# Optimization experiments

Hardware: AMD Instinct MI355X
Metric: run time of the kernel (lower is better)

Reference implementation:

```python
import jax, jax.numpy as jnp
import numpy as np

DN = ('NCHW', 'OIHW', 'NCHW')
A, NC = 3, 80  # num_anchors, num_classes


def conv(x, w, b, pad=1):
    y = jax.lax.conv_general_dilated(x, w, (1, 1), [(pad, pad), (pad, pad)], dimension_numbers=DN)
    return y + b[None, :, None, None]


def up2(x):
    return jnp.repeat(jnp.repeat(x, 2, axis=2), 2, axis=3)


def gen_anchors():
    # AnchorGenerator: sizes per level, 3 aspect ratios, 1 scale, stride=2**(i+3)
    sizes = [32.0, 64.0, 128.0]
    ars = [0.5, 1.0, 2.0]
    hw = [(64, 64), (32, 32), (16, 16)]
    out = []
    for i, ((h, w), bs) in enumerate(zip(hw, sizes)):
        stride = 2.0 ** (i + 3)
        base = np.array([[-bs * np.sqrt(a) / 2, -bs / np.sqrt(a) / 2,
                          bs * np.sqrt(a) / 2, bs / np.sqrt(a) / 2] for a in ars], dtype=np.float32)
        sx = np.arange(w, dtype=np.float32) * stride
        sy = np.arange(h, dtype=np.float32) * stride
        yy, xx = np.meshgrid(sy, sx, indexing='ij')  # torch.meshgrid default 'ij'
        shifts = np.stack([xx.ravel(), yy.ravel(), xx.ravel(), yy.ravel()], axis=1)
        anc = (base[None, :, :] + shifts[:, None, :]).reshape(-1, 4)
        out.append(anc)
    return jnp.asarray(np.concatenate(out, axis=0))


def setup_inputs() -> dict:
    key = jax.random.key(0)
    ks = jax.random.split(key, 32)
    def w(k, o, i, kh, kw):
        return jax.random.normal(k, (o, i, kh, kw), jnp.float32) * 0.02
    B = 8
    inp = {
        'feat3': jax.random.normal(ks[0], (B, 512, 64, 64), jnp.float32),
        'feat4': jax.random.normal(ks[1], (B, 1024, 32, 32), jnp.float32),
        'feat5': jax.random.normal(ks[2], (B, 2048, 16, 16), jnp.float32),
        # FPN lateral 1x1 convs
        'lw0': w(ks[3], 256, 512, 1, 1),  'lb0': jnp.zeros(256, jnp.float32),
        'lw1': w(ks[4], 256, 1024, 1, 1), 'lb1': jnp.zeros(256, jnp.float32),
        'lw2': w(ks[5], 256, 2048, 1, 1), 'lb2': jnp.zeros(256, jnp.float32),
        # FPN 3x3 output convs
        'fw0': w(ks[6], 256, 256, 3, 3), 'fb0': jnp.zeros(256, jnp.float32),
        'fw1': w(ks[7], 256, 256, 3, 3), 'fb1': jnp.zeros(256, jnp.float32),
        'fw2': w(ks[8], 256, 256, 3, 3), 'fb2': jnp.zeros(256, jnp.float32),
        # cls tower (shared across levels)
        'cw0': w(ks[9], 256, 256, 3, 3),  'cb0': jnp.zeros(256, jnp.float32),
        'cw1': w(ks[10], 256, 256, 3, 3), 'cb1': jnp.zeros(256, jnp.float32),
        'cw2': w(ks[11], A * NC, 256, 3, 3), 'cb2': jnp.zeros(A * NC, jnp.float32),
        # reg tower (shared across levels)
        'rw0': w(ks[12], 256, 256, 3, 3), 'rb0': jnp.zeros(256, jnp.float32),
        'rw1': w(ks[13], 256, 256, 3, 3), 'rb1': jnp.zeros(256, jnp.float32),
        'rw2': w(ks[14], A * 4, 256, 3, 3), 'rb2': jnp.zeros(A * 4, jnp.float32),
    }
    return inp


def _tower(f, w0, b0, w1, b1, w2, b2):
    x = jax.nn.relu(conv(f, w0, b0))
    x = jax.nn.relu(conv(x, w1, b1))
    return conv(x, w2, b2)


def reference(feat3, feat4, feat5,
              lw0, lb0, lw1, lb1, lw2, lb2,
              fw0, fb0, fw1, fb1, fw2, fb2,
              cw0, cb0, cw1, cb1, cw2, cb2,
              rw0, rb0, rw1, rb1, rw2, rb2):
    B = feat3.shape[0]
    # FPN: lateral 1x1 convs + top-down nearest upsample fusion + 3x3 convs
    l0 = conv(feat3, lw0, lb0, pad=0)
    l1 = conv(feat4, lw1, lb1, pad=0)
    l2 = conv(feat5, lw2, lb2, pad=0)
    l1 = l1 + up2(l2)
    l0 = l0 + up2(l1)
    feats = [conv(l0, fw0, fb0), conv(l1, fw1, fb1), conv(l2, fw2, fb2)]
    cls_list, reg_list = [], []
    for f in feats:
        c = _tower(f, cw0, cb0, cw1, cb1, cw2, cb2)  # [B, A*NC, H, W]
        r = _tower(f, rw0, rb0, rw1, rb1, rw2, rb2)  # [B, A*4, H, W]
        H, W = c.shape[2], c.shape[3]
        # view(B, A, C, HW).permute(0, 3, 1, 2) -> [B, HW, A, C]
        c = c.reshape(B, A, NC, H * W).transpose(0, 3, 1, 2)
        r = r.reshape(B, A, 4, H * W).transpose(0, 3, 1, 2)
        cls_list.append(c.reshape(B, H * W, A * NC))
        reg_list.append(r.reshape(B, H * W, A * 4))
    cls_all = jnp.concatenate(cls_list, axis=1)   # [B, 5376, 240]
    reg_all = jnp.concatenate(reg_list, axis=1)   # [B, 5376, 12]
    out = jnp.concatenate([cls_all, reg_all], axis=-1)  # [B, 5376, 252]
    anchors = gen_anchors()  # [16128, 4]
    return out, anchors
```

## Files before the change

### kernel.cpp

```cpp
#include <hip/hip_runtime.h>

typedef __bf16 bf16_t;
typedef __bf16 bf16x8 __attribute__((ext_vector_type(8)));
typedef float f32x4 __attribute__((ext_vector_type(4)));

__device__ inline void gl_lds16(const bf16_t* g, bf16_t* l) {
  __builtin_amdgcn_global_load_lds(
      (const __attribute__((address_space(1))) void*)g,
      (__attribute__((address_space(3))) void*)l, 16, 0, 0);
}

__global__ __launch_bounds__(256)
void nchw_to_nhwc(const float* __restrict__ in, bf16_t* __restrict__ out,
                  int C, int HW) {
  __shared__ float tile[64][65];
  const int n = blockIdx.z;
  const int c0 = blockIdx.y * 64, p0 = blockIdx.x * 64;
  const int t = threadIdx.x;
  const float* src = in + ((size_t)n * C + c0) * HW + p0;
  const int cl = t >> 6;
  const int pl = t & 63;
#pragma unroll
  for (int i = 0; i < 16; ++i)
    tile[cl + i * 4][pl] = src[(size_t)(cl + i * 4) * HW + pl];
  __syncthreads();
  bf16_t* dst = out + ((size_t)n * HW + p0) * C + c0;
  const int pc = t >> 6;
  const int cc = t & 63;
#pragma unroll
  for (int i = 0; i < 16; ++i)
    dst[(size_t)(pc + i * 4) * C + cc] = (bf16_t)tile[cc][pc + i * 4];
}

struct WSrc {
  const float *lw0, *lw1, *lw2;
  const float* w9[9];
  int O9[9];
};
__global__ __launch_bounds__(256)
void weight_prep(WSrc s, bf16_t* __restrict__ LWT0, bf16_t* __restrict__ LWT1,
                 bf16_t* __restrict__ LWT2, bf16_t* __restrict__ W33) {
  int idx = blockIdx.x * 256 + threadIdx.x;
  if (idx < 131072) { LWT0[idx] = (bf16_t)s.lw0[idx]; return; }
  if (idx < 393216) { int i = idx - 131072; LWT1[i] = (bf16_t)s.lw1[i]; return; }
  if (idx < 917504) { int i = idx - 393216; LWT2[i] = (bf16_t)s.lw2[i]; return; }
  int t2 = idx - 917504;
  if (t2 >= 9 * 589824) return;
  int sgi = t2 / 589824;
  int r = t2 - sgi * 589824;
  int kid = r >> 16;
  int rem = r & 65535;
  int o = rem >> 8, ci = rem & 255;
  const float* src = s.w9[sgi];
  int O = s.O9[sgi];
  W33[t2] = (o < O) ? (bf16_t)src[((size_t)o * 256 + ci) * 9 + kid] : (bf16_t)0.0f;
}

__global__ __launch_bounds__(256)
void up2_add_p(bf16_t* __restrict__ dst, const bf16_t* __restrict__ src,
               int lw, int lhw, int dWp, int dNs, int sWp, int sNs, int tot8) {
  int idx = blockIdx.x * 256 + threadIdx.x;
  if (idx >= tot8) return;
  const int c8 = idx & 31;
  const int pos = idx >> 5;
  const int n = pos >> lhw;
  const int rem = pos & ((1 << lhw) - 1);
  const int y = rem >> lw, x = rem & ((1 << lw) - 1);
  bf16_t* d = dst + ((size_t)n * dNs + (y + 1) * dWp + (x + 1)) * 256 + c8 * 8;
  const bf16_t* sp = src + ((size_t)n * sNs + ((y >> 1) + 1) * sWp + ((x >> 1) + 1)) * 256 + c8 * 8;
  bf16x8 dv = *(bf16x8*)d;
  bf16x8 sv = *(const bf16x8*)sp;
#pragma unroll
  for (int k = 0; k < 8; ++k) dv[k] = (bf16_t)((float)dv[k] + (float)sv[k]);
  *(bf16x8*)d = dv;
}

struct Job1 {
  const bf16_t* A;
  const bf16_t* Wt;
  const float* bias;
  bf16_t* outb;
  int mtiles, lw, lhw, oWp, onstride, Cin, pad0, pad1;
};
struct Job1Pack { Job1 j[3]; };

__global__ __launch_bounds__(256, 2)
void conv1_batch(Job1Pack jp) {
  __shared__ __align__(16) bf16_t As[2][128 * 32];
  __shared__ __align__(16) bf16_t Bs[2][128 * 32];
  int b = blockIdx.x, ji = 0;
#pragma unroll 1
  for (; ji < 2; ++ji) {
    int sz = jp.j[ji].mtiles * 2;
    if (b < sz) break;
    b -= sz;
  }
  const Job1 J = jp.j[ji];
  const int nt = b & 1, mt = b >> 1;
  const int m0 = mt * 128, n0 = nt * 128;
  const int t = threadIdx.x, l = t & 63, w = t >> 6;
  const int W = 1 << J.lw, HW = 1 << J.lhw;
  const int sr = l >> 2, seg = (l & 3) * 8;
  const bf16_t* aptr[2];
  const bf16_t* bptr[2];
  int lrow[2];
#pragma unroll
  for (int q = 0; q < 2; ++q) {
    const int r = w * 32 + q * 16 + sr;
    aptr[q] = J.A + (size_t)(m0 + r) * J.Cin + seg;
    bptr[q] = J.Wt + (size_t)(n0 + r) * J.Cin + seg;
    lrow[q] = (w * 32 + q * 16) * 32;
  }
  const int fr = l & 15, qd = l >> 4;
  const int wm = (w & 1) * 64, wn = (w >> 1) * 64;

  f32x4 acc[4][4];
#pragma unroll
  for (int i = 0; i < 4; ++i)
#pragma unroll
    for (int j = 0; j < 4; ++j)
#pragma unroll
      for (int r = 0; r < 4; ++r) acc[i][j][r] = 0.0f;

  auto stage = [&](int buf, int kk) {
#pragma unroll
    for (int q = 0; q < 2; ++q) {
      gl_lds16(aptr[q] + (size_t)kk * 32, &As[buf][lrow[q]]);
      gl_lds16(bptr[q] + (size_t)kk * 32, &Bs[buf][lrow[q]]);
    }
  };

  stage(0, 0);

  const int kiters = J.Cin >> 5;
#pragma unroll 1
  for (int kk = 0; kk < kiters; ++kk) {
    const int cur = kk & 1;
    __syncthreads();
    if (kk + 1 < kiters) stage(cur ^ 1, kk + 1);
    bf16x8 af[4], bfv[4];
#pragma unroll
    for (int i = 0; i < 4; ++i)
      af[i] = *(const bf16x8*)&As[cur][(wm + i * 16 + fr) * 32 + qd * 8];
#pragma unroll
    for (int j = 0; j < 4; ++j)
      bfv[j] = *(const bf16x8*)&Bs[cur][(wn + j * 16 + fr) * 32 + qd * 8];
#pragma unroll
    for (int i = 0; i < 4; ++i)
#pragma unroll
      for (int j = 0; j < 4; ++j)
        acc[i][j] = __builtin_amdgcn_mfma_f32_16x16x32_bf16(af[i], bfv[j],
                                                            acc[i][j], 0, 0, 0);
  }

#pragma unroll
  for (int i = 0; i < 4; ++i) {
    const int mrow = m0 + wm + i * 16 + qd * 4;
#pragma unroll
    for (int j = 0; j < 4; ++j) {
      const int co = n0 + wn + j * 16 + fr;
      const float bv = J.bias[co];
#pragma unroll
      for (int r = 0; r < 4; ++r) {
        float v = acc[i][j][r] + bv;
        const int m = mrow + r;
        const int n = m >> J.lhw, hw = m & (HW - 1);
        const int y = hw >> J.lw, x = hw & (W - 1);
        J.outb[((size_t)n * J.onstride + (y + 1) * J.oWp + (x + 1)) * 256 + co] =
            (bf16_t)v;
      }
    }
  }
}

struct Job3 {
  const bf16_t* A;
  const bf16_t* Wt;
  const float* bias;
  bf16_t* outb;
  int mtiles, ntiles, lw, lhw, Wp, nsA, oWp, onstride;
  int relu, Cout, pos_off, ch_off, use_outf, nAr, Pc, pad_;
};
struct Job3Pack { Job3 j[6]; };

__global__ __launch_bounds__(256, 2)
void conv3_batch(Job3Pack jp, float* __restrict__ outf) {
  __shared__ __align__(16) bf16_t As[320 * 32];
  __shared__ __align__(16) bf16_t Bs[2][384 * 32];
  int b = blockIdx.x, ji = 0;
#pragma unroll 1
  for (; ji < 5; ++ji) {
    int sz = jp.j[ji].mtiles * jp.j[ji].ntiles;
    if (b < sz) break;
    b -= sz;
  }
  const Job3 J = jp.j[ji];
  const int nt = (J.ntiles == 2) ? (b & 1) : 0;
  const int mt = (J.ntiles == 2) ? (b >> 1) : b;
  const int m0 = mt * 128, n0 = nt * 128;
  const int t = threadIdx.x, l = t & 63, w = t >> 6;
  const int W = 1 << J.lw, HW = 1 << J.lhw;
  const int sr = l >> 2, seg = (l & 3) * 8;
  const int fr = l & 15, qd = l >> 4;
  const int wm = (w & 1) * 64, wn = (w >> 1) * 64;
  const int wrow = w * 16 + sr;

  const int n_img = m0 >> J.lhw;
  const int Y0 = (m0 & (HW - 1)) >> J.lw;
  const bf16_t* Ag = J.A + ((size_t)n_img * J.nsA + (size_t)Y0 * J.Wp) * 256;

  int apix[4];
#pragma unroll
  for (int i = 0; i < 4; ++i) {
    const int m = wm + i * 16 + fr;
    const int y = m >> J.lw, x = m & (W - 1);
    apix[i] = ((y + 1) * J.Wp + (x + 1)) * 32 + qd * 8;
  }

  f32x4 acc[4][4];
#pragma unroll
  for (int i = 0; i < 4; ++i)
#pragma unroll
    for (int j = 0; j < 4; ++j)
#pragma unroll
      for (int r = 0; r < 4; ++r) acc[i][j][r] = 0.0f;

  auto stageB = [&](int buf, int ky, int cboff) {
#pragma unroll
    for (int r = 0; r < 6; ++r) {
      const int R = r * 64 + wrow;
      const int tp = R >> 7, co = R & 127;
      gl_lds16(J.Wt + (size_t)(ky * 3 + tp) * 65536 +
                   (size_t)(n0 + co) * 256 + cboff + seg,
               &Bs[buf][(r * 64 + w * 16) * 32]);
    }
  };
  auto stageA = [&](int cboff) {
#pragma unroll 1
    for (int r = 0; r < J.nAr; ++r) {
      int p = r * 64 + wrow;
      p = (p < J.Pc) ? p : (J.Pc - 1);
      gl_lds16(Ag + (size_t)p * 256 + cboff + seg,
               &As[(r * 64 + w * 16) * 32]);
    }
  };

  stageA(0);
  stageB(0, 0, 0);

  int cb = 0, ky = 0;
#pragma unroll 1
  for (int p = 0; p < 24; ++p) {
    const int cur = p & 1;
    __syncthreads();
    if (p < 23) {
      int kyn = ky + 1, cbn = cb;
      if (kyn == 3) { kyn = 0; cbn = cb + 1; }
      stageB(cur ^ 1, kyn, cbn * 32);
    }
    const bool aB = (ky == 2) && (cb < 7);
    const int dyoff = (ky - 1) * J.Wp * 32;
#pragma unroll
    for (int kx = 0; kx < 3; ++kx) {
      const int d = dyoff + (kx - 1) * 32;
      bf16x8 af[4], bfv[4];
#pragma unroll
      for (int i = 0; i < 4; ++i)
        af[i] = *(const bf16x8*)&As[apix[i] + d];
#pragma unroll
      for (int j = 0; j < 4; ++j)
        bfv[j] = *(const bf16x8*)&Bs[cur][(kx * 128 + wn + j * 16 + fr) * 32 + qd * 8];
      if (kx == 2 && aB) {
        asm volatile("s_waitcnt lgkmcnt(0)" ::: "memory");
        __builtin_amdgcn_sched_barrier(0);
        __builtin_amdgcn_s_barrier();
        __builtin_amdgcn_sched_barrier(0);
        stageA((cb + 1) * 32);
      }
#pragma unroll
      for (int i = 0; i < 4; ++i)
#pragma unroll
        for (int j = 0; j < 4; ++j)
          acc[i][j] = __builtin_amdgcn_mfma_f32_16x16x32_bf16(af[i], bfv[j],
                                                              acc[i][j], 0, 0, 0);
    }
    ky = (ky == 2) ? 0 : ky + 1;
    if (ky == 0) ++cb;
  }

#pragma unroll
  for (int i = 0; i < 4; ++i) {
    const int mrow = m0 + wm + i * 16 + qd * 4;
#pragma unroll
    for (int j = 0; j < 4; ++j) {
      const int co = n0 + wn + j * 16 + fr;
      if (co < J.Cout) {
        const float bv = J.bias[co];
#pragma unroll
        for (int r = 0; r < 4; ++r) {
          float v = acc[i][j][r] + bv;
          if (J.relu) v = fmaxf(v, 0.0f);
          const int m = mrow + r;
          const int n = m >> J.lhw, hw = m & (HW - 1);
          if (J.use_outf) {
            outf[((size_t)n * 5376 + J.pos_off + hw) * 252 + J.ch_off + co] = v;
          } else {
            const int y = hw >> J.lw, x = hw & (W - 1);
            J.outb[((size_t)n * J.onstride + (y + 1) * J.oWp + (x + 1)) * 256 + co] =
                (bf16_t)v;
          }
        }
      }
    }
  }
}

__global__ __launch_bounds__(256)
void anchors_k(float* __restrict__ out) {
  int r = blockIdx.x * 256 + threadIdx.x;
  if (r >= 16128) return;
  int local, w, stride;
  float bs;
  if (r < 12288)      { local = r;          w = 64; stride = 8;  bs = 32.f;  }
  else if (r < 15360) { local = r - 12288;  w = 32; stride = 16; bs = 64.f;  }
  else                { local = r - 15360;  w = 16; stride = 32; bs = 128.f; }
  const int a = local % 3;
  const int s = local / 3;
  const int y = s / w, x = s - y * w;
  const float ar = (a == 0) ? 0.5f : (a == 1) ? 1.0f : 2.0f;
  const float sq = sqrtf(ar);
  const float hw_ = bs * sq * 0.5f, hh = bs / sq * 0.5f;
  const float cx = (float)x * (float)stride, cy = (float)y * (float)stride;
  out[(size_t)r * 4 + 0] = cx - hw_;
  out[(size_t)r * 4 + 1] = cy - hh;
  out[(size_t)r * 4 + 2] = cx + hw_;
  out[(size_t)r * 4 + 3] = cy + hh;
}

extern "C" void kernel_launch(void* const* d_in, const int* in_sizes, int n_in,
                              void* d_out, int out_size, void* d_ws, size_t ws_size,
                              hipStream_t stream) {
  const float* feat3 = (const float*)d_in[0];
  const float* feat4 = (const float*)d_in[1];
  const float* feat5 = (const float*)d_in[2];
  const float* lw0 = (const float*)d_in[3];  const float* lb0 = (const float*)d_in[4];
  const float* lw1 = (const float*)d_in[5];  const float* lb1 = (const float*)d_in[6];
  const float* lw2 = (const float*)d_in[7];  const float* lb2 = (const float*)d_in[8];
  const float* fw0 = (const float*)d_in[9];  const float* fb0 = (const float*)d_in[10];
  const float* fw1 = (const float*)d_in[11]; const float* fb1 = (const float*)d_in[12];
  const float* fw2 = (const float*)d_in[13]; const float* fb2 = (const float*)d_in[14];
  const float* cw0 = (const float*)d_in[15]; const float* cb0 = (const float*)d_in[16];
  const float* cw1 = (const float*)d_in[17]; const float* cb1 = (const float*)d_in[18];
  const float* cw2 = (const float*)d_in[19]; const float* cb2 = (const float*)d_in[20];
  const float* rw0 = (const float*)d_in[21]; const float* rb0 = (const float*)d_in[22];
  const float* rw1 = (const float*)d_in[23]; const float* rb1 = (const float*)d_in[24];
  const float* rw2 = (const float*)d_in[25]; const float* rb2 = (const float*)d_in[26];

  char* ws = (char*)d_ws;
  float* out = (float*)d_out;

  bf16_t* XS3 = (bf16_t*)(ws + 0);
  bf16_t* XS4 = (bf16_t*)(ws + 33554432);
  bf16_t* XS5 = (bf16_t*)(ws + 50331648);
  bf16_t* Lp0 = (bf16_t*)(ws + 58720256);
  bf16_t* Lp1 = (bf16_t*)(ws + 76562432);
  bf16_t* Lp2 = (bf16_t*)(ws + 81297408);
  bf16_t* Pp0 = (bf16_t*)(ws + 82624512);
  bf16_t* Pp1 = (bf16_t*)(ws + 100466688);
  bf16_t* Pp2 = (bf16_t*)(ws + 105201664);
  bf16_t* LWT0 = (bf16_t*)(ws + 106528768);
  bf16_t* LWT1 = (bf16_t*)(ws + 106790912);
  bf16_t* LWT2 = (bf16_t*)(ws + 107315200);
  bf16_t* W33  = (bf16_t*)(ws + 108363776);
  bf16_t* FWT0 = W33 + 0 * 589824;
  bf16_t* FWT1 = W33 + 1 * 589824;
  bf16_t* FWT2 = W33 + 2 * 589824;
  bf16_t* CWT0 = W33 + 3 * 589824;
  bf16_t* CWT1 = W33 + 4 * 589824;
  bf16_t* CWT2 = W33 + 5 * 589824;
  bf16_t* RWT0 = W33 + 6 * 589824;
  bf16_t* RWT1 = W33 + 7 * 589824;
  bf16_t* RWT2 = W33 + 8 * 589824;
  bf16_t* TAc0 = (bf16_t*)(ws + 0);
  bf16_t* TAr0 = (bf16_t*)(ws + 17842176);
  bf16_t* TAc1 = (bf16_t*)(ws + 35684352);
  bf16_t* TAr1 = (bf16_t*)(ws + 40419328);
  bf16_t* TAc2 = (bf16_t*)(ws + 45154304);
  bf16_t* TAr2 = (bf16_t*)(ws + 46481408);
  bf16_t* TBc0 = Pp0; bf16_t* TBr0 = Lp0;
  bf16_t* TBc1 = Pp1; bf16_t* TBr1 = Lp1;
  bf16_t* TBc2 = Pp2; bf16_t* TBr2 = Lp2;

  WSrc wsrc;
  wsrc.lw0 = lw0; wsrc.lw1 = lw1; wsrc.lw2 = lw2;
  const float* w9s[9] = {fw0, fw1, fw2, cw0, cw1, cw2, rw0, rw1, rw2};
  int o9s[9] = {256, 256, 256, 256, 256, 240, 256, 256, 12};
  for (int i = 0; i < 9; ++i) { wsrc.w9[i] = w9s[i]; wsrc.O9[i] = o9s[i]; }
  weight_prep<<<dim3(24320), 256, 0, stream>>>(wsrc, LWT0, LWT1, LWT2, W33);

  nchw_to_nhwc<<<dim3(64, 8, 8),  256, 0, stream>>>(feat3, XS3, 512, 4096);
  nchw_to_nhwc<<<dim3(16, 16, 8), 256, 0, stream>>>(feat4, XS4, 1024, 1024);
  nchw_to_nhwc<<<dim3(4, 32, 8),  256, 0, stream>>>(feat5, XS5, 2048, 256);

  hipMemsetAsync(ws + 58720256, 0, 47808512, stream);

  {
    Job1Pack jp;
    jp.j[0] = {XS3, LWT0, lb0, Lp0, 256, 6, 12, 66, 4356, 512, 0, 0};
    jp.j[1] = {XS4, LWT1, lb1, Lp1, 64, 5, 10, 34, 1156, 1024, 0, 0};
    jp.j[2] = {XS5, LWT2, lb2, Lp2, 16, 4, 8, 18, 324, 2048, 0, 0};
    conv1_batch<<<dim3(672), 256, 0, stream>>>(jp);
  }

  hipMemsetAsync(ws + 0, 0, 47808512, stream);

  up2_add_p<<<dim3(1024), 256, 0, stream>>>(Lp1, Lp2, 5, 10, 34, 1156, 18, 324, 262144);
  up2_add_p<<<dim3(4096), 256, 0, stream>>>(Lp0, Lp1, 6, 12, 66, 4356, 34, 1156, 1048576);

  auto mk3 = [](const bf16_t* A, const bf16_t* Wt, const float* bias,
                bf16_t* outb, int mtiles, int ntiles, int lw, int lhw,
                int Wp, int nsA, int oWp, int onstride, int relu, int Cout,
                int pos_off, int ch_off, int use_outf, int nAr, int Pc) {
    Job3 j;
    j.A = A; j.Wt = Wt; j.bias = bias; j.outb = outb;
    j.mtiles = mtiles; j.ntiles = ntiles; j.lw = lw; j.lhw = lhw;
    j.Wp = Wp; j.nsA = nsA; j.oWp = oWp; j.onstride = onstride;
    j.relu = relu; j.Cout = Cout; j.pos_off = pos_off; j.ch_off = ch_off;
    j.use_outf = use_outf; j.nAr = nAr; j.Pc = Pc; j.pad_ = 0;
    return j;
  };

  {
    Job3Pack jp;
    jp.j[0] = mk3(Lp0, FWT0, fb0, Pp0, 256, 2, 6, 12, 66, 4356, 66, 4356, 0, 256, 0, 0, 0, 5, 264);
    jp.j[1] = mk3(Lp1, FWT1, fb1, Pp1, 64, 2, 5, 10, 34, 1156, 34, 1156, 0, 256, 0, 0, 0, 4, 204);
    jp.j[2] = mk3(Lp2, FWT2, fb2, Pp2, 16, 2, 4, 8, 18, 324, 18, 324, 0, 256, 0, 0, 0, 3, 180);
    jp.j[3] = jp.j[4] = jp.j[5] = jp.j[2];
    jp.j[3].mtiles = jp.j[4].mtiles = jp.j[5].mtiles = 0;
    conv3_batch<<<dim3(672), 256, 0, stream>>>(jp, out);
  }

  {
    Job3Pack jp;
    jp.j[0] = mk3(Pp0, CWT0, cb0, TAc0, 256, 2, 6, 12, 66, 4356, 66, 4356, 1, 256, 0, 0, 0, 5, 264);
    jp.j[1] = mk3(Pp0, RWT0, rb0, TAr0, 256, 2, 6, 12, 66, 4356, 66, 4356, 1, 256, 0, 0, 0, 5, 264);
    jp.j[2] = mk3(Pp1, CWT0, cb0, TAc1, 64, 2, 5, 10, 34, 1156, 34, 1156, 1, 256, 0, 0, 0, 4, 204);
    jp.j[3] = mk3(Pp1, RWT0, rb0, TAr1, 64, 2, 5, 10, 34, 1156, 34, 1156, 1, 256, 0, 0, 0, 4, 204);
    jp.j[4] = mk3(Pp2, CWT0, cb0, TAc2, 16, 2, 4, 8, 18, 324, 18, 324, 1, 256, 0, 0, 0, 3, 180);
    jp.j[5] = mk3(Pp2, RWT0, rb0, TAr2, 16, 2, 4, 8, 18, 324, 18, 324, 1, 256, 0, 0, 0, 3, 180);
    conv3_batch<<<dim3(1344), 256, 0, stream>>>(jp, out);
  }

  {
    Job3Pack jp;
    jp.j[0] = mk3(TAc0, CWT1, cb1, TBc0, 256, 2, 6, 12, 66, 4356, 66, 4356, 1, 256, 0, 0, 0, 5, 264);
    jp.j[1] = mk3(TAr0, RWT1, rb1, TBr0, 256, 2, 6, 12, 66, 4356, 66, 4356, 1, 256, 0, 0, 0, 5, 264);
    jp.j[2] = mk3(TAc1, CWT1, cb1, TBc1, 64, 2, 5, 10, 34, 1156, 34, 1156, 1, 256, 0, 0, 0, 4, 204);
    jp.j[3] = mk3(TAr1, RWT1, rb1, TBr1, 64, 2, 5, 10, 34, 1156, 34, 1156, 1, 256, 0, 0, 0, 4, 204);
    jp.j[4] = mk3(TAc2, CWT1, cb1, TBc2, 16, 2, 4, 8, 18, 324, 18, 324, 1, 256, 0, 0, 0, 3, 180);
    jp.j[5] = mk3(TAr2, RWT1, rb1, TBr2, 16, 2, 4, 8, 18, 324, 18, 324, 1, 256, 0, 0, 0, 3, 180);
    conv3_batch<<<dim3(1344), 256, 0, stream>>>(jp, out);
  }

  {
    Job3Pack jp;
    jp.j[0] = mk3(TBc0, CWT2, cb2, nullptr, 256, 2, 6, 12, 66, 4356, 0, 0, 0, 240, 0, 0, 1, 5, 264);
    jp.j[1] = mk3(TBr0, RWT2, rb2, nullptr, 256, 1, 6, 12, 66, 4356, 0, 0, 0, 12, 0, 240, 1, 5, 264);
    jp.j[2] = mk3(TBc1, CWT2, cb2, nullptr, 64, 2, 5, 10, 34, 1156, 0, 0, 0, 240, 4096, 0, 1, 4, 204);
    jp.j[3] = mk3(TBr1, RWT2, rb2, nullptr, 64, 1, 5, 10, 34, 1156, 0, 0, 0, 12, 4096, 240, 1, 4, 204);
    jp.j[4] = mk3(TBc2, CWT2, cb2, nullptr, 16, 2, 4, 8, 18, 324, 0, 0, 0, 240, 5120, 0, 1, 3, 180);
    jp.j[5] = mk3(TBr2, RWT2, rb2, nullptr, 16, 1, 4, 8, 18, 324, 0, 0, 0, 12, 5120, 240, 1, 3, 180);
    conv3_batch<<<dim3(1008), 256, 0, stream>>>(jp, out);
  }

  anchors_k<<<dim3(63), 256, 0, stream>>>(out + 10838016);
}
```

Before: 723.4 us.

## Stage one tap per buffer with XOR-swizzled LDS and higher occupancy

```diff
diff --git a/kernel.cpp b/kernel.cpp
--- a/kernel.cpp
+++ b/kernel.cpp
@@ -183,10 +183,10 @@
 };
 struct Job3Pack { Job3 j[6]; };
 
-__global__ __launch_bounds__(256, 2)
+__global__ __launch_bounds__(256, 4)
 void conv3_batch(Job3Pack jp, float* __restrict__ outf) {
   __shared__ __align__(16) bf16_t As[320 * 32];
-  __shared__ __align__(16) bf16_t Bs[2][384 * 32];
+  __shared__ __align__(16) bf16_t Bs[2][128 * 32];
   int b = blockIdx.x, ji = 0;
 #pragma unroll 1
   for (; ji < 5; ++ji) {
@@ -200,7 +200,8 @@
   const int m0 = mt * 128, n0 = nt * 128;
   const int t = threadIdx.x, l = t & 63, w = t >> 6;
   const int W = 1 << J.lw, HW = 1 << J.lhw;
-  const int sr = l >> 2, seg = (l & 3) * 8;
+  const int sr = l >> 2;
+  const int segsw = (((l & 3) ^ (sr & 3)) << 3);
   const int fr = l & 15, qd = l >> 4;
   const int wm = (w & 1) * 64, wn = (w >> 1) * 64;
   const int wrow = w * 16 + sr;
@@ -209,13 +210,14 @@
   const int Y0 = (m0 & (HW - 1)) >> J.lw;
   const bf16_t* Ag = J.A + ((size_t)n_img * J.nsA + (size_t)Y0 * J.Wp) * 256;
 
-  int apix[4];
+  int api[4];
 #pragma unroll
   for (int i = 0; i < 4; ++i) {
     const int m = wm + i * 16 + fr;
     const int y = m >> J.lw, x = m & (W - 1);
-    apix[i] = ((y + 1) * J.Wp + (x + 1)) * 32 + qd * 8;
-  }
+    api[i] = (y + 1) * J.Wp + (x + 1);
+  }
+  const int qsB = ((qd ^ (fr & 3)) << 3);
 
   f32x4 acc[4][4];
 #pragma unroll
@@ -225,22 +227,18 @@
 #pragma unroll
       for (int r = 0; r < 4; ++r) acc[i][j][r] = 0.0f;
 
-  auto stageB = [&](int buf, int ky, int cboff) {
-#pragma unroll
-    for (int r = 0; r < 6; ++r) {
-      const int R = r * 64 + wrow;
-      const int tp = R >> 7, co = R & 127;
-      gl_lds16(J.Wt + (size_t)(ky * 3 + tp) * 65536 +
-                   (size_t)(n0 + co) * 256 + cboff + seg,
-               &Bs[buf][(r * 64 + w * 16) * 32]);
-    }
+  const bf16_t* Bgl = J.Wt + (size_t)(n0 + wrow) * 256 + segsw;
+  auto stageB = [&](int buf, int tapIdx, int cboff) {
+    const bf16_t* src = Bgl + (size_t)tapIdx * 65536 + cboff;
+    gl_lds16(src, &Bs[buf][(w * 16) * 32]);
+    gl_lds16(src + 64 * 256, &Bs[buf][(64 + w * 16) * 32]);
   };
   auto stageA = [&](int cboff) {
 #pragma unroll 1
     for (int r = 0; r < J.nAr; ++r) {
       int p = r * 64 + wrow;
       p = (p < J.Pc) ? p : (J.Pc - 1);
-      gl_lds16(Ag + (size_t)p * 256 + cboff + seg,
+      gl_lds16(Ag + (size_t)p * 256 + cboff + segsw,
                &As[(r * 64 + w * 16) * 32]);
     }
   };
@@ -248,44 +246,46 @@
   stageA(0);
   stageB(0, 0, 0);
 
-  int cb = 0, ky = 0;
-#pragma unroll 1
-  for (int p = 0; p < 24; ++p) {
-    const int cur = p & 1;
-    __syncthreads();
-    if (p < 23) {
-      int kyn = ky + 1, cbn = cb;
-      if (kyn == 3) { kyn = 0; cbn = cb + 1; }
-      stageB(cur ^ 1, kyn, cbn * 32);
+  int buf = 0;
+#pragma unroll 1
+  for (int cb = 0; cb < 8; ++cb) {
+#pragma unroll 1
+    for (int ky = 0; ky < 3; ++ky) {
+      const int dyp = (ky - 1) * J.Wp;
+#pragma unroll
+      for (int kx = 0; kx < 3; ++kx) {
+        __syncthreads();
+        {
+          int tn = ky * 3 + kx + 1, cbn = cb;
+          if (tn == 9) { tn = 0; cbn = cb + 1; }
+          if (cbn < 8) stageB(buf ^ 1, tn, cbn * 32);
+        }
+        const int dpix = dyp + (kx - 1);
+        bf16x8 af[4], bfv[4];
+#pragma unroll
+        for (int i = 0; i < 4; ++i) {
+          const int pix = api[i] + dpix;
+          af[i] = *(const bf16x8*)&As[pix * 32 + ((qd ^ (pix & 3)) << 3)];
+        }
+#pragma unroll
+        for (int j = 0; j < 4; ++j)
+          bfv[j] = *(const bf16x8*)&Bs[buf][(wn + j * 16 + fr) * 32 + qsB];
+        if (ky == 2 && kx == 2 && cb < 7) {
+          asm volatile("s_waitcnt lgkmcnt(0)" ::: "memory");
+          __builtin_amdgcn_sched_barrier(0);
+          __builtin_amdgcn_s_barrier();
+          __builtin_amdgcn_sched_barrier(0);
+          stageA((cb + 1) * 32);
+        }
+#pragma unroll
+        for (int i = 0; i < 4; ++i)
+#pragma unroll
+          for (int j = 0; j < 4; ++j)
+            acc[i][j] = __builtin_amdgcn_mfma_f32_16x16x32_bf16(af[i], bfv[j],
+                                                                acc[i][j], 0, 0, 0);
+        buf ^= 1;
+      }
     }
-    const bool aB = (ky == 2) && (cb < 7);
-    const int dyoff = (ky - 1) * J.Wp * 32;
-#pragma unroll
-    for (int kx = 0; kx < 3; ++kx) {
-      const int d = dyoff + (kx - 1) * 32;
-      bf16x8 af[4], bfv[4];
-#pragma unroll
-      for (int i = 0; i < 4; ++i)
-        af[i] = *(const bf16x8*)&As[apix[i] + d];
-#pragma unroll
-      for (int j = 0; j < 4; ++j)
-        bfv[j] = *(const bf16x8*)&Bs[cur][(kx * 128 + wn + j * 16 + fr) * 32 + qd * 8];
-      if (kx == 2 && aB) {
-        asm volatile("s_waitcnt lgkmcnt(0)" ::: "memory");
-        __builtin_amdgcn_sched_barrier(0);
-        __builtin_amdgcn_s_barrier();
-        __builtin_amdgcn_sched_barrier(0);
-        stageA((cb + 1) * 32);
-      }
-#pragma unroll
-      for (int i = 0; i < 4; ++i)
-#pragma unroll
-        for (int j = 0; j < 4; ++j)
-          acc[i][j] = __builtin_amdgcn_mfma_f32_16x16x32_bf16(af[i], bfv[j],
-                                                              acc[i][j], 0, 0, 0);
-    }
-    ky = (ky == 2) ? 0 : ky + 1;
-    if (ky == 0) ++cb;
   }
 
 #pragma unroll
```

New measurement: 901.8 us. 1.25x slower.
